# Performance work log

Hardware: AMD Instinct MI355X
Metric: run time of the kernel (lower is better)

Reference implementation:

```python
import jax, jax.numpy as jnp
import numpy as np

N_EXPERTS = 8
D_IN = 1024
D_OUT = 1024
BATCH = 4096


def setup_inputs() -> dict:
    key = jax.random.key(0)
    k_x, k_w, k_b, k_a = jax.random.split(key, 4)
    xs = jax.random.normal(k_x, (BATCH, D_IN), dtype=jnp.float32)
    mxs = jnp.arange(BATCH, dtype=jnp.int32)  # opaque per-sample metadata, passed through
    actions = jax.random.randint(k_a, (BATCH,), 0, N_EXPERTS, dtype=jnp.int64)
    # Expert parameters: each submodule is Linear(D_IN -> D_OUT)
    W = jax.random.normal(k_w, (N_EXPERTS, D_OUT, D_IN), dtype=jnp.float32) / np.sqrt(D_IN)
    b = jax.random.normal(k_b, (N_EXPERTS, D_OUT), dtype=jnp.float32) * 0.01
    return {"xs": xs, "mxs": mxs, "actions": actions, "W": W, "b": b}


def reference(xs, mxs, actions, W, b):
    # Original: per-sample python loop y_i = submodule[actions[i]](x_i); cat along batch.
    # Vectorized: compute all experts densely (E small), then select per-sample row.
    y_all = jnp.einsum("bj,eij->bei", xs, W) + b[None, :, :]  # [B, E, D_OUT]
    ys = jnp.take_along_axis(y_all, actions[:, None, None].astype(jnp.int32), axis=1)
    ys = jnp.squeeze(ys, axis=1)  # [B, D_OUT]
    return (ys, mxs, actions)
```

## Files before the change

kernel.cpp:

```cpp
#include <hip/hip_runtime.h>

#define BATCH 4096
#define D_IN 1024
#define D_OUT 1024
#define N_EXPERTS 8

#define TM 64
#define TN 128
#define TK 32
#define MAX_TILES 71

#define WS_PERM    0
#define WS_STARTS  4096
#define WS_TILE_E  4112
#define WS_TILE_M  4200
#define WS_NTILES  4288

typedef __attribute__((ext_vector_type(8))) short short8;
typedef __attribute__((ext_vector_type(4))) float f32x4;

__global__ void group_kernel(const int* __restrict__ actions, int* __restrict__ ws) {
    __shared__ int cnt[N_EXPERTS];
    __shared__ int base[N_EXPERTS];
    const int t = threadIdx.x;
    if (t < N_EXPERTS) cnt[t] = 0;
    __syncthreads();
    for (int i = t; i < BATCH; i += 256) atomicAdd(&cnt[actions[i]], 1);
    __syncthreads();
    if (t == 0) {
        int s = 0, nt = 0;
        for (int e = 0; e < N_EXPERTS; ++e) {
            const int c = cnt[e];
            base[e] = s;
            ws[WS_STARTS + e] = s;
            for (int m0 = 0; m0 < c; m0 += TM) {
                ws[WS_TILE_E + nt] = e;
                ws[WS_TILE_M + nt] = m0;
                ++nt;
            }
            s += c;
            cnt[e] = 0;
        }
        ws[WS_STARTS + N_EXPERTS] = s;
        ws[WS_NTILES] = nt;
    }
    __syncthreads();
    for (int i = t; i < BATCH; i += 256) {
        const int a = actions[i];
        const int pos = base[a] + atomicAdd(&cnt[a], 1);
        ws[WS_PERM + pos] = i;
    }
}

__device__ __forceinline__ void cvt8(const float4 a, const float4 b,
                                     short8& h, short8& l) {
    float f[8] = {a.x, a.y, a.z, a.w, b.x, b.y, b.z, b.w};
#pragma unroll
    for (int i = 0; i < 8; ++i) {
        const unsigned u = __float_as_uint(f[i]);
        h[i] = (short)(u >> 16);
        const float r = f[i] - __uint_as_float(u & 0xffff0000u);
        l[i] = (short)(__float_as_uint(r) >> 16);
    }
}

__global__ __launch_bounds__(256) void moe_gemm(
    const float* __restrict__ xs, const float* __restrict__ W,
    const float* __restrict__ bias, const int* __restrict__ ws,
    float* __restrict__ out)
{
    const int tix = blockIdx.y;
    if (tix >= ws[WS_NTILES]) return;
    const int e   = ws[WS_TILE_E + tix];
    const int m0  = ws[WS_TILE_M + tix];
    const int s0  = ws[WS_STARTS + e];
    const int cnt = ws[WS_STARTS + e + 1] - s0;
    const int n0  = blockIdx.x * TN;

    __shared__ short Ahi[TM * TK];
    __shared__ short Alo[TM * TK];
    __shared__ short Bhi[TN * TK];
    __shared__ short Blo[TN * TK];
    __shared__ int   rows_s[TM];

    const int t = threadIdx.x;
    if (t < TM) {
        const int r = m0 + t;
        rows_s[t] = (r < cnt) ? ws[WS_PERM + s0 + r] : -1;
    }
    __syncthreads();

    const int lane = t & 63;
    const int wave = t >> 6;
    const int wm = (wave & 1) * 32;
    const int wn = (wave >> 1) * 64;

    const float zf = 0.f;
    f32x4 acc[2][4];
#pragma unroll
    for (int mi = 0; mi < 2; ++mi)
#pragma unroll
        for (int nj = 0; nj < 4; ++nj)
            acc[mi][nj] = (f32x4){zf, zf, zf, zf};

    const float* Wb = W + (size_t)e * (D_OUT * (size_t)D_IN) + (size_t)n0 * D_IN;

    const int j  = t & 3;
    const int rr = t >> 2;

    const int arow = rows_s[rr];
    const float* aptr = (arow >= 0) ? (xs + (size_t)arow * D_IN + j * 8) : nullptr;
    const int aoff_st = (rr >> 4) * 512 + (j * 16 + (rr & 15)) * 8;

    for (int k0 = 0; k0 < D_IN; k0 += TK) {
        __syncthreads();
        {
            float4 v0 = make_float4(0.f, 0.f, 0.f, 0.f), v1 = v0;
            if (aptr) {
                v0 = *(const float4*)(aptr + k0);
                v1 = *(const float4*)(aptr + k0 + 4);
            }
            short8 h, l;
            cvt8(v0, v1, h, l);
            *(short8*)&Ahi[aoff_st] = h;
            *(short8*)&Alo[aoff_st] = l;
        }
#pragma unroll
        for (int i = 0; i < 2; ++i) {
            const int n   = i * 64 + rr;
            const int off = (n >> 4) * 512 + (j * 16 + (n & 15)) * 8;
            const float* q = Wb + (size_t)n * D_IN + k0 + j * 8;
            const float4 w0 = *(const float4*)q;
            const float4 w1 = *(const float4*)(q + 4);
            short8 h, l;
            cvt8(w0, w1, h, l);
            *(short8*)&Bhi[off] = h;
            *(short8*)&Blo[off] = l;
        }
        __syncthreads();

        short8 ah[2], al[2], bh[4], bl[4];
#pragma unroll
        for (int i2 = 0; i2 < 2; ++i2) {
            const int aoff = ((wm >> 4) + i2) * 512 + lane * 8;
            ah[i2] = *(const short8*)&Ahi[aoff];
            al[i2] = *(const short8*)&Alo[aoff];
        }
#pragma unroll
        for (int i2 = 0; i2 < 4; ++i2) {
            const int boff = ((wn >> 4) + i2) * 512 + lane * 8;
            bh[i2] = *(const short8*)&Bhi[boff];
            bl[i2] = *(const short8*)&Blo[boff];
        }
#pragma unroll
        for (int mi = 0; mi < 2; ++mi)
#pragma unroll
            for (int nj = 0; nj < 4; ++nj) {
                acc[mi][nj] = __builtin_amdgcn_mfma_f32_16x16x32_bf16(ah[mi], bh[nj], acc[mi][nj], 0, 0, 0);
                acc[mi][nj] = __builtin_amdgcn_mfma_f32_16x16x32_bf16(ah[mi], bl[nj], acc[mi][nj], 0, 0, 0);
                acc[mi][nj] = __builtin_amdgcn_mfma_f32_16x16x32_bf16(al[mi], bh[nj], acc[mi][nj], 0, 0, 0);
            }
    }

    const int cl = lane & 15;
    const int qd = lane >> 4;
    float bv[4];
#pragma unroll
    for (int nj = 0; nj < 4; ++nj)
        bv[nj] = bias[e * D_OUT + n0 + wn + nj * 16 + cl];
#pragma unroll
    for (int mi = 0; mi < 2; ++mi) {
#pragma unroll
        for (int reg = 0; reg < 4; ++reg) {
            const int mloc = wm + mi * 16 + qd * 4 + reg;
            const int r = rows_s[mloc];
            if (r >= 0) {
                float* orow = out + (size_t)r * D_OUT + n0 + wn + cl;
#pragma unroll
                for (int nj = 0; nj < 4; ++nj)
                    orow[nj * 16] = acc[mi][nj][reg] + bv[nj];
            }
        }
    }
}

__global__ void meta_float_kernel(const int* __restrict__ mxs,
                                  const int* __restrict__ actions,
                                  float* __restrict__ out) {
    const int i = blockIdx.x * 256 + threadIdx.x;
    if (i < BATCH) {
        out[BATCH * D_OUT + i] = (float)mxs[i];
        out[BATCH * D_OUT + BATCH + i] = (float)actions[i];
    }
}

__global__ void meta_raw64_kernel(const int* __restrict__ mxs,
                                  const int* __restrict__ actions,
                                  float* __restrict__ out) {
    const int i = blockIdx.x * 256 + threadIdx.x;
    if (i < BATCH) {
        out[BATCH * D_OUT + i] = (float)mxs[i];
        long long* a64 = (long long*)(out + BATCH * D_OUT + BATCH);
        a64[i] = (long long)actions[i];
    }
}

extern "C" void kernel_launch(void* const* d_in, const int* in_sizes, int n_in,
                              void* d_out, int out_size, void* d_ws, size_t ws_size,
                              hipStream_t stream) {
    const float* xs      = (const float*)d_in[0];
    const int*   mxs     = (const int*)d_in[1];
    const int*   actions = (const int*)d_in[2];
    const float* W       = (const float*)d_in[3];
    const float* bias    = (const float*)d_in[4];
    float* out = (float*)d_out;
    int*   ws  = (int*)d_ws;

    group_kernel<<<1, 256, 0, stream>>>(actions, ws);

    dim3 grid(D_OUT / TN, MAX_TILES, 1);
    moe_gemm<<<grid, 256, 0, stream>>>(xs, W, bias, ws, out);

    const int metaOff = BATCH * D_OUT;
    if (out_size >= metaOff + 3 * BATCH) {
        meta_raw64_kernel<<<(BATCH + 255) / 256, 256, 0, stream>>>(mxs, actions, out);
    } else if (out_size >= metaOff + 2 * BATCH) {
        meta_float_kernel<<<(BATCH + 255) / 256, 256, 0, stream>>>(mxs, actions, out);
    }
}
```

Measured before the change: 155.1 us.

## Prefetch next K-tile into registers and XOR-swizzle LDS slots

Global loads for the next K tile of xs and W are issued into registers right after the LDS barrier, so they overlap with the LDS reads and MFMA work of the current tile. The LDS store and read offsets get an XOR swizzle on the slot index to cut bank conflicts. The leading __syncthreads is replaced by a raw s_barrier at the end of each iteration. This raises register pressure, and the raw barrier needs correct ordering of LDS reads against the next iteration's writes.

Result: faster. 145.0 us (-6.5%).

```diff
diff --git a/kernel.cpp b/kernel.cpp
--- a/kernel.cpp
+++ b/kernel.cpp
@@ -110,45 +110,57 @@
 
     const int arow = rows_s[rr];
     const float* aptr = (arow >= 0) ? (xs + (size_t)arow * D_IN + j * 8) : nullptr;
-    const int aoff_st = (rr >> 4) * 512 + (j * 16 + (rr & 15)) * 8;
-
-    for (int k0 = 0; k0 < D_IN; k0 += TK) {
-        __syncthreads();
+
+    const int slotA   = (j * 16 + (rr & 15)) ^ (j << 1);
+    const int aoff_st = (rr >> 4) * 512 + slotA * 8;
+    const int boff0   = aoff_st;
+    const int boff1   = aoff_st + 4 * 512;
+
+    const float* qb0 = Wb + (size_t)rr * D_IN + j * 8;
+    const float* qb1 = Wb + (size_t)(64 + rr) * D_IN + j * 8;
+
+    const int rds = (lane ^ ((lane >> 4) << 1)) * 8;
+
+    float4 ra0 = make_float4(0.f, 0.f, 0.f, 0.f), ra1 = ra0;
+    if (aptr) { ra0 = *(const float4*)(aptr);     ra1 = *(const float4*)(aptr + 4); }
+    float4 rb0 = *(const float4*)(qb0),           rb1 = *(const float4*)(qb0 + 4);
+    float4 rb2 = *(const float4*)(qb1),           rb3 = *(const float4*)(qb1 + 4);
+
+    for (int k0 = 0; ; ) {
         {
-            float4 v0 = make_float4(0.f, 0.f, 0.f, 0.f), v1 = v0;
-            if (aptr) {
-                v0 = *(const float4*)(aptr + k0);
-                v1 = *(const float4*)(aptr + k0 + 4);
-            }
             short8 h, l;
-            cvt8(v0, v1, h, l);
+            cvt8(ra0, ra1, h, l);
             *(short8*)&Ahi[aoff_st] = h;
             *(short8*)&Alo[aoff_st] = l;
-        }
-#pragma unroll
-        for (int i = 0; i < 2; ++i) {
-            const int n   = i * 64 + rr;
-            const int off = (n >> 4) * 512 + (j * 16 + (n & 15)) * 8;
-            const float* q = Wb + (size_t)n * D_IN + k0 + j * 8;
-            const float4 w0 = *(const float4*)q;
-            const float4 w1 = *(const float4*)(q + 4);
-            short8 h, l;
-            cvt8(w0, w1, h, l);
-            *(short8*)&Bhi[off] = h;
-            *(short8*)&Blo[off] = l;
+            cvt8(rb0, rb1, h, l);
+            *(short8*)&Bhi[boff0] = h;
+            *(short8*)&Blo[boff0] = l;
+            cvt8(rb2, rb3, h, l);
+            *(short8*)&Bhi[boff1] = h;
+            *(short8*)&Blo[boff1] = l;
         }
         __syncthreads();
 
+        const int kn = k0 + TK;
+        if (kn < D_IN) {
+            if (aptr) {
+                ra0 = *(const float4*)(aptr + kn);
+                ra1 = *(const float4*)(aptr + kn + 4);
+            }
+            rb0 = *(const float4*)(qb0 + kn); rb1 = *(const float4*)(qb0 + kn + 4);
+            rb2 = *(const float4*)(qb1 + kn); rb3 = *(const float4*)(qb1 + kn + 4);
+        }
+
         short8 ah[2], al[2], bh[4], bl[4];
 #pragma unroll
         for (int i2 = 0; i2 < 2; ++i2) {
-            const int aoff = ((wm >> 4) + i2) * 512 + lane * 8;
+            const int aoff = ((wm >> 4) + i2) * 512 + rds;
             ah[i2] = *(const short8*)&Ahi[aoff];
             al[i2] = *(const short8*)&Alo[aoff];
         }
 #pragma unroll
         for (int i2 = 0; i2 < 4; ++i2) {
-            const int boff = ((wn >> 4) + i2) * 512 + lane * 8;
+            const int boff = ((wn >> 4) + i2) * 512 + rds;
             bh[i2] = *(const short8*)&Bhi[boff];
             bl[i2] = *(const short8*)&Blo[boff];
         }
@@ -160,6 +172,10 @@
                 acc[mi][nj] = __builtin_amdgcn_mfma_f32_16x16x32_bf16(ah[mi], bl[nj], acc[mi][nj], 0, 0, 0);
                 acc[mi][nj] = __builtin_amdgcn_mfma_f32_16x16x32_bf16(al[mi], bh[nj], acc[mi][nj], 0, 0, 0);
             }
+
+        if (kn >= D_IN) break;
+        k0 = kn;
+        asm volatile("s_barrier" ::: "memory");
     }
 
     const int cl = lane & 15;
```
